# Kernel optimization log

Hardware: AMD Instinct MI355X
Metric: run time of the kernel (lower is better)

Reference implementation:

```python
import jax, jax.numpy as jnp
import numpy as np

N_HEAD = 16

def setup_inputs() -> dict:
    key = jax.random.key(0)
    ks = jax.random.split(key, 5)
    B, T, C = 4, 1024, 1024
    d = C // N_HEAD
    x = jax.random.normal(ks[0], (B, T, C), dtype=jnp.float32)
    w_attn = jax.random.normal(ks[1], (C, 3 * C), dtype=jnp.float32) * 0.02
    w_proj = jax.random.normal(ks[2], (C, C), dtype=jnp.float32) * 0.02
    embk = 0.02 * jax.random.normal(ks[3], (T, d), dtype=jnp.float32)
    embv = 0.02 * jax.random.normal(ks[4], (T, d), dtype=jnp.float32)
    return {"x": x, "w_attn": w_attn, "w_proj": w_proj, "embk": embk, "embv": embv}

def reference(x, w_attn, w_proj, embk, embv):
    B, T, C = x.shape
    H = N_HEAD
    d = C // H
    qkv = x @ w_attn                                   # [B,T,3C]
    q, k, v = jnp.split(qkv, 3, axis=2)
    q = q.reshape(B, T, H, d).transpose(0, 2, 1, 3)     # [B,H,T,d]
    k = k.reshape(B, T, H, d).transpose(0, 2, 1, 3)
    v = v.reshape(B, T, H, d).transpose(0, 2, 1, 3)
    # relative positions, lower-triangular (0 above diagonal, masked anyway)
    idx = jnp.arange(T)
    rel = jnp.tril(idx[:, None] - idx[None, :])         # [T,T] int
    rk = embk[rel]                                      # [T,T,d]
    rv = embv[rel]                                      # [T,T,d]
    scale = 1.0 / np.sqrt(d).astype(np.float32)
    att = jnp.einsum('bhtd,bhsd->bhts', q, k) * scale \
        + jnp.einsum('bhtd,tsd->bhts', q, rk)           # [B,H,T,T]
    causal = (idx[None, :] <= idx[:, None])             # [T,T] bool
    att = jnp.where(causal[None, None], att, -jnp.inf)
    att = jax.nn.softmax(att, axis=-1)
    y = jnp.einsum('bhts,bhsd->bhtd', att, v) \
      + jnp.einsum('bhts,tsd->bhtd', att, rv)           # [B,H,T,d]
    y = y.transpose(0, 2, 1, 3).reshape(B, T, C)
    return y @ w_proj
```

## Files before the change

kernel.cpp:

```cpp
#include <hip/hip_runtime.h>
#include <math.h>

typedef unsigned short u16;
typedef short bf8 __attribute__((ext_vector_type(8)));
typedef float f32x4 __attribute__((ext_vector_type(4)));

__device__ __forceinline__ u16 f2b(float f) {
    union { float f; unsigned u; } x; x.f = f;
    return (u16)((x.u + 0x7FFFu + ((x.u >> 16) & 1u)) >> 16);
}
__device__ __forceinline__ float b2f(u16 b) {
    union { unsigned u; float f; } x; x.u = ((unsigned)b) << 16;
    return x.f;
}

__device__ __forceinline__ void async16(const void* g, void* l) {
    __builtin_amdgcn_global_load_lds(
        (const __attribute__((address_space(1))) unsigned int*)g,
        (__attribute__((address_space(3))) unsigned int*)l, 16, 0, 0);
}

__device__ __forceinline__ void cstore(float* p, float v) { *p = v; }
__device__ __forceinline__ void cstore(u16* p, float v) { *p = f2b(v); }

template<typename OutT>
__global__ __launch_bounds__(256) void gemm_mfma(const u16* __restrict__ A,
                                                 const u16* __restrict__ Bt,
                                                 OutT* __restrict__ C,
                                                 int M, int N, int K) {
    __shared__ __align__(16) u16 As[128 * 32];
    __shared__ __align__(16) u16 Bs[128 * 32];
    const int tid = threadIdx.x;
    const int w = tid >> 6, L = tid & 63;
    const int l15 = L & 15, quad = L >> 4;
    const int wm = (w >> 1) * 64, wn = (w & 1) * 64;
    const int row0 = blockIdx.y * 128, col0 = blockIdx.x * 128;
    const int laneRow = L >> 2, laneCol8 = (L & 3) * 8;

    f32x4 acc[4][4] = {};

    for (int k0 = 0; k0 < K; k0 += 32) {
        #pragma unroll
        for (int i = 0; i < 2; ++i) {
            const int seg = w * 2 + i;
            const int r = seg * 16 + laneRow;
            async16(&A[(size_t)(row0 + r) * K + k0 + laneCol8], &As[seg * 512 + L * 8]);
        }
        #pragma unroll
        for (int i = 0; i < 2; ++i) {
            const int seg = w * 2 + i;
            const int r = seg * 16 + laneRow;
            async16(&Bt[(size_t)(col0 + r) * K + k0 + laneCol8], &Bs[seg * 512 + L * 8]);
        }
        __syncthreads();
        bf8 a[4], b[4];
        #pragma unroll
        for (int mt = 0; mt < 4; ++mt)
            a[mt] = *(const bf8*)&As[(wm + mt * 16 + l15) * 32 + quad * 8];
        #pragma unroll
        for (int nt = 0; nt < 4; ++nt)
            b[nt] = *(const bf8*)&Bs[(wn + nt * 16 + l15) * 32 + quad * 8];
        #pragma unroll
        for (int mt = 0; mt < 4; ++mt)
            #pragma unroll
            for (int nt = 0; nt < 4; ++nt)
                acc[mt][nt] = __builtin_amdgcn_mfma_f32_16x16x32_bf16(
                    a[mt], b[nt], acc[mt][nt], 0, 0, 0);
        __syncthreads();
    }
    #pragma unroll
    for (int mt = 0; mt < 4; ++mt)
        #pragma unroll
        for (int nt = 0; nt < 4; ++nt) {
            const int col = col0 + wn + nt * 16 + l15;
            #pragma unroll
            for (int r = 0; r < 4; ++r) {
                const int row = row0 + wm + mt * 16 + quad * 4 + r;
                cstore(&C[(size_t)row * N + col], acc[mt][nt][r]);
            }
        }
}

__global__ __launch_bounds__(256) void prep_all(const float* __restrict__ x,
                                                const float* __restrict__ embk,
                                                const float* __restrict__ embv,
                                                const float* __restrict__ w_attn,
                                                const float* __restrict__ w_proj,
                                                u16* __restrict__ xb,
                                                u16* __restrict__ EKP,
                                                u16* __restrict__ EVP,
                                                u16* __restrict__ waT,
                                                u16* __restrict__ wpT) {
    __shared__ u16 ts[64][65];
    const int bx = blockIdx.x;
    const int tid = threadIdx.x;
    if (bx < 4096) {
        int idx = bx * 256 + tid;
        const float4 v = ((const float4*)x)[idx];
        ((ushort4*)xb)[idx] = make_ushort4(f2b(v.x), f2b(v.y), f2b(v.z), f2b(v.w));
    } else if (bx < 4132) {
        int t = (bx - 4096) * 256 + tid;
        int L = t & 63, kc = (t >> 6) & 1, k16 = t >> 7;
        int l15 = L & 15, quad = L >> 4;
        int row = 1 + k16 * 16 + l15;
        int d = row - 128;
        int cl = d < 0 ? 0 : (d > 1023 ? 1023 : d);
        const float* p = embk + cl * 64 + kc * 32 + quad * 8;
        #pragma unroll
        for (int i = 0; i < 8; ++i) EKP[t * 8 + i] = f2b(p[i]);
    } else if (bx < 4168) {
        int t = (bx - 4132) * 256 + tid;
        int L = t & 63, rest = t >> 6;
        int c32 = rest % 36, tn = rest / 36;
        int l15 = L & 15, quad = L >> 4;
        #pragma unroll
        for (int i = 0; i < 8; ++i) {
            int c = c32 * 32 + quad * 8 + i;
            int d = c - 127;
            int cl = d < 0 ? 0 : (d > 1023 ? 1023 : d);
            EVP[t * 8 + i] = f2b(embv[cl * 64 + tn * 16 + l15]);
        }
    } else {
        const float* W; u16* WT; int Cc, t;
        if (bx < 4168 + 768) { t = bx - 4168; W = w_attn; WT = waT; Cc = 3072; }
        else                 { t = bx - 4936; W = w_proj; WT = wpT; Cc = 1024; }
        const int nx = Cc >> 6;
        const int c0 = (t % nx) * 64, r0 = (t / nx) * 64;
        for (int i = tid; i < 4096; i += 256) {
            int r = i >> 6, c = i & 63;
            ts[r][c] = f2b(W[(size_t)(r0 + r) * Cc + c0 + c]);
        }
        __syncthreads();
        for (int i = tid; i < 4096; i += 256) {
            int c = i >> 6, r = i & 63;
            WT[(size_t)(c0 + c) * 1024 + r0 + r] = ts[r][c];
        }
    }
}

__global__ __launch_bounds__(256) void prep_vt(const u16* __restrict__ qkvb,
                                               u16* __restrict__ Vt) {
    __shared__ u16 ts[64][65];
    const int tid = threadIdx.x;
    const int s0 = blockIdx.x * 64;
    const int bh = blockIdx.y, b = bh >> 4, h = bh & 15;
    #pragma unroll
    for (int it = 0; it < 4; ++it) {
        int s = it * 16 + (tid >> 4);
        int d4 = (tid & 15) * 4;
        const u16* p = qkvb + (size_t)(b * 1024 + s0 + s) * 3072 + 2048 + h * 64 + d4;
        #pragma unroll
        for (int i = 0; i < 4; ++i) ts[s][d4 + i] = p[i];
    }
    __syncthreads();
    const int d = tid >> 2, si = (tid & 3) * 16;
    __align__(16) u16 buf[16];
    #pragma unroll
    for (int i = 0; i < 16; ++i) buf[i] = ts[si + i][d];
    u16* o = Vt + ((size_t)(bh * 64 + d) << 10) + s0 + si;
    *(uint4*)o       = ((uint4*)buf)[0];
    *(uint4*)(o + 8) = ((uint4*)buf)[1];
}

__global__ __launch_bounds__(256) void pack_kv(const u16* __restrict__ qkvb,
                                               const u16* __restrict__ Vt,
                                               u16* __restrict__ Kp,
                                               u16* __restrict__ Vp) {
    const int bx = blockIdx.x;
    if (bx < 2048) {
        int t = bx * 256 + threadIdx.x;
        int L = t & 63, kc = (t >> 6) & 1, s16 = (t >> 7) & 63, bh = t >> 13;
        int l15 = L & 15, quad = L >> 4;
        int b = bh >> 4, h = bh & 15;
        const u16* src = qkvb + (size_t)(b * 1024 + s16 * 16 + l15) * 3072
                       + 1024 + h * 64 + kc * 32 + quad * 8;
        u16* dst = Kp + (size_t)t * 8;
        #pragma unroll
        for (int i = 0; i < 8; ++i) dst[i] = f2b(b2f(src[i]) * 0.125f);
    } else {
        int t = (bx - 2048) * 256 + threadIdx.x;
        int L = t & 63, c32 = (t >> 6) & 31, tn = (t >> 11) & 3, bh = t >> 13;
        int l15 = L & 15, quad = L >> 4;
        const u16* src = Vt + ((size_t)(bh * 64 + tn * 16 + l15) << 10)
                       + c32 * 32 + quad * 8;
        *(uint4*)(Vp + (size_t)t * 8) = *(const uint4*)src;
    }
}

__global__ __launch_bounds__(256) void attn_mfma(const u16* __restrict__ qkvb,
                                                 const u16* __restrict__ Kp,
                                                 const u16* __restrict__ Vp,
                                                 const u16* __restrict__ EKP,
                                                 const u16* __restrict__ EVP,
                                                 u16* __restrict__ yb) {
    __shared__ __align__(16) u16 slab_[4][4608];
    __shared__ __align__(16) u16 KVs[16384];

    const int tid = threadIdx.x;
    const int w = tid >> 6, L = tid & 63;
    const int l15 = L & 15, quad = L >> 4;
    const int pair = blockIdx.x;
    const int bh = blockIdx.y, b = bh >> 4, h = bh & 15;
    u16* S2l = slab_[w];
    u16* Pl  = slab_[w];
    u16* Ppl = slab_[w] + 2048;

    const bf8* EKPF = (const bf8*)EKP;
    const bf8* EVPF = (const bf8*)EVP;

    #pragma unroll 1
    for (int half = 0; half < 2; ++half) {
        const int tile = half ? pair : (15 - pair);
        const int t0 = tile * 64;

        bf8 qn[2];
        {
            const int trow = t0 + w * 16 + l15;
            const u16* qp = qkvb + (size_t)(b * 1024 + trow) * 3072 + h * 64 + quad * 8;
            qn[0] = *(const bf8*)qp;
            qn[1] = *(const bf8*)(qp + 32);
        }

        f32x4 o[4] = {};
        float lsum[4] = {0.f, 0.f, 0.f, 0.f};

        const int nch = (t0 >> 7) + 1;
        #pragma unroll 1
        for (int c = 0; c < nch; ++c) {
            const int s0 = c << 7;
            const int diff = t0 - s0;

            __syncthreads();

            {
                const size_t kbase = ((size_t)(bh * 64 + (s0 >> 4)) << 1) * 512;
                #pragma unroll
                for (int i = 0; i < 4; ++i)
                    async16(Kp + kbase + (i * 256 + tid) * 8, &KVs[(i * 256 + tid) * 8]);
                const int vb = bh * 128 + (s0 >> 5);
                #pragma unroll
                for (int i = 0; i < 4; ++i)
                    async16(Vp + ((size_t)(vb + i * 32) * 512 + tid * 8),
                            &KVs[8192 + i * 2048 + tid * 8]);
            }

            f32x4 s2[9] = {};
            {
                const int kb = (diff >> 4) + w;
                #pragma unroll
                for (int j = 0; j < 9; ++j) {
                    #pragma unroll
                    for (int kc = 0; kc < 2; ++kc)
                        s2[j] = __builtin_amdgcn_mfma_f32_16x16x32_bf16(
                            qn[kc], EKPF[(((kb + j) << 1) + kc) * 64 + L], s2[j], 0, 0, 0);
                }
            }
            #pragma unroll
            for (int j = 0; j < 9; ++j)
                #pragma unroll
                for (int r = 0; r < 4; ++r)
                    S2l[(quad * 4 + r) * 148 + j * 16 + l15] = f2b(s2[j][r]);

            __syncthreads();

            f32x4 s1[8] = {};
            #pragma unroll
            for (int tn = 0; tn < 8; ++tn) {
                #pragma unroll
                for (int kc = 0; kc < 2; ++kc) {
                    const bf8 kf = *(const bf8*)&KVs[((tn << 1) + kc) * 512 + L * 8];
                    s1[tn] = __builtin_amdgcn_mfma_f32_16x16x32_bf16(
                        qn[kc], kf, s1[tn], 0, 0, 0);
                }
            }

            #pragma unroll
            for (int tn = 0; tn < 8; ++tn) {
                const int cl = tn * 16 + l15;
                #pragma unroll
                for (int r = 0; r < 4; ++r) {
                    const int row = quad * 4 + r;
                    float v = s1[tn][r] + b2f(S2l[row * 148 + (row - cl + 127)]);
                    if (cl > diff + w * 16 + row) v = -1e30f;
                    float p = __expf(v - 4.0f);
                    s1[tn][r] = p;
                    lsum[r] += p;
                }
            }
            #pragma unroll
            for (int i = 0; i < 5; ++i)
                ((uint4*)Ppl)[i * 64 + L] = make_uint4(0, 0, 0, 0);
            #pragma unroll
            for (int tn = 0; tn < 8; ++tn) {
                const int cl = tn * 16 + l15;
                #pragma unroll
                for (int r = 0; r < 4; ++r) {
                    const int row = quad * 4 + r;
                    const u16 pb = f2b(s1[tn][r]);
                    Pl[((cl >> 5) << 9) + (((cl >> 3) & 3) << 7) + (row << 3) + (cl & 7)] = pb;
                    const int dc = (w & 1) * 16 + row - cl + 127;
                    Ppl[((dc >> 5) << 9) + (((dc >> 3) & 3) << 7) + (row << 3) + (dc & 7)] = pb;
                }
            }

            {
                bf8 pa[4];
                #pragma unroll
                for (int kc = 0; kc < 4; ++kc) pa[kc] = ((const bf8*)Pl)[kc * 64 + L];
                #pragma unroll
                for (int tn = 0; tn < 4; ++tn) {
                    #pragma unroll
                    for (int kc = 0; kc < 4; ++kc) {
                        const bf8 vf = *(const bf8*)&KVs[8192 + (tn * 4 + kc) * 512 + L * 8];
                        o[tn] = __builtin_amdgcn_mfma_f32_16x16x32_bf16(
                            pa[kc], vf, o[tn], 0, 0, 0);
                    }
                }
            }
            {
                bf8 pa[5];
                #pragma unroll
                for (int kc = 0; kc < 5; ++kc) pa[kc] = ((const bf8*)Ppl)[kc * 64 + L];
                const int eb = (diff >> 5) + (w >> 1);
                #pragma unroll
                for (int tn = 0; tn < 4; ++tn) {
                    #pragma unroll
                    for (int kc = 0; kc < 5; ++kc)
                        o[tn] = __builtin_amdgcn_mfma_f32_16x16x32_bf16(
                            pa[kc], EVPF[(tn * 36 + eb + kc) * 64 + L], o[tn], 0, 0, 0);
                }
            }
        }
        #pragma unroll
        for (int r = 0; r < 4; ++r) {
            float ls = lsum[r];
            ls += __shfl_xor(ls, 1); ls += __shfl_xor(ls, 2);
            ls += __shfl_xor(ls, 4); ls += __shfl_xor(ls, 8);
            lsum[r] = ls;
        }
        #pragma unroll
        for (int tn = 0; tn < 4; ++tn) {
            const int col = h * 64 + tn * 16 + l15;
            #pragma unroll
            for (int r = 0; r < 4; ++r) {
                const int trow = t0 + w * 16 + quad * 4 + r;
                yb[(size_t)(b * 1024 + trow) * 1024 + col] = f2b(o[tn][r] / lsum[r]);
            }
        }
    }
}

extern "C" void kernel_launch(void* const* d_in, const int* in_sizes, int n_in,
                              void* d_out, int out_size, void* d_ws, size_t ws_size,
                              hipStream_t stream) {
    const float* x      = (const float*)d_in[0];
    const float* w_attn = (const float*)d_in[1];
    const float* w_proj = (const float*)d_in[2];
    const float* embk   = (const float*)d_in[3];
    const float* embv   = (const float*)d_in[4];
    float* out = (float*)d_out;

    u16* wsb   = (u16*)d_ws;
    u16* qkvb  = wsb;
    u16* xb    = qkvb + 12582912;
    u16* ymidb = xb;
    u16* waT   = xb + 4194304;
    u16* wpT   = waT + 3145728;
    u16* Vt    = wpT + 1048576;
    u16* Kp    = Vt + 4194304;
    u16* Vp    = Kp + 4194304;
    u16* EKP   = Vp + 4194304;
    u16* EVP   = EKP + 73728;

    prep_all<<<dim3(5192), 256, 0, stream>>>(x, embk, embv, w_attn, w_proj,
                                             xb, EKP, EVP, waT, wpT);
    gemm_mfma<u16><<<dim3(24, 32), 256, 0, stream>>>(xb, waT, qkvb, 4096, 3072, 1024);
    prep_vt<<<dim3(16, 64), 256, 0, stream>>>(qkvb, Vt);
    pack_kv<<<dim3(4096), 256, 0, stream>>>(qkvb, Vt, Kp, Vp);
    attn_mfma<<<dim3(8, 64), 256, 0, stream>>>(qkvb, Kp, Vp, EKP, EVP, ymidb);
    gemm_mfma<float><<<dim3(8, 32), 256, 0, stream>>>(ymidb, wpT, out, 4096, 1024, 1024);
}
```

Baseline: 275.8 us.

## Fuse V transpose into pack_kv, use bpermute for rel-pos scores, skip masked diagonal MFMAs

Merges the prep_vt and pack_kv kernels into one that transposes V through LDS and writes the MFMA-packed Vp directly. This removes one launch and the Vt intermediate round trip through global memory. In the attention kernel, the relative-position score gather now uses ds_bpermute on registers instead of a bf16 round trip through an LDS slab, which also drops a rounding step. On diagonal chunks, MFMAs covering fully masked tiles are skipped, and the Ppl zeroing is hoisted out of the loop, with some added branching.

```diff
diff --git a/kernel.cpp b/kernel.cpp
--- a/kernel.cpp
+++ b/kernel.cpp
@@ -138,52 +138,49 @@
     }
 }
 
-__global__ __launch_bounds__(256) void prep_vt(const u16* __restrict__ qkvb,
-                                               u16* __restrict__ Vt) {
-    __shared__ u16 ts[64][65];
-    const int tid = threadIdx.x;
-    const int s0 = blockIdx.x * 64;
-    const int bh = blockIdx.y, b = bh >> 4, h = bh & 15;
-    #pragma unroll
-    for (int it = 0; it < 4; ++it) {
-        int s = it * 16 + (tid >> 4);
-        int d4 = (tid & 15) * 4;
-        const u16* p = qkvb + (size_t)(b * 1024 + s0 + s) * 3072 + 2048 + h * 64 + d4;
-        #pragma unroll
-        for (int i = 0; i < 4; ++i) ts[s][d4 + i] = p[i];
-    }
-    __syncthreads();
-    const int d = tid >> 2, si = (tid & 3) * 16;
-    __align__(16) u16 buf[16];
-    #pragma unroll
-    for (int i = 0; i < 16; ++i) buf[i] = ts[si + i][d];
-    u16* o = Vt + ((size_t)(bh * 64 + d) << 10) + s0 + si;
-    *(uint4*)o       = ((uint4*)buf)[0];
-    *(uint4*)(o + 8) = ((uint4*)buf)[1];
-}
-
 __global__ __launch_bounds__(256) void pack_kv(const u16* __restrict__ qkvb,
-                                               const u16* __restrict__ Vt,
                                                u16* __restrict__ Kp,
                                                u16* __restrict__ Vp) {
-    const int bx = blockIdx.x;
-    if (bx < 2048) {
-        int t = bx * 256 + threadIdx.x;
-        int L = t & 63, kc = (t >> 6) & 1, s16 = (t >> 7) & 63, bh = t >> 13;
-        int l15 = L & 15, quad = L >> 4;
-        int b = bh >> 4, h = bh & 15;
+    __shared__ __align__(16) u16 ts[128][72];
+    const int tid = threadIdx.x;
+    const int sb = blockIdx.x;
+    const int bh = blockIdx.y, b = bh >> 4, h = bh & 15;
+    const int s0 = sb * 128;
+    const int L = tid & 63, fr0 = tid >> 6;
+    const int l15 = L & 15, quad = L >> 4;
+
+    #pragma unroll
+    for (int it = 0; it < 2; ++it) {
+        const int row = it * 64 + (tid >> 2);
+        const int c16 = (tid & 3) * 16;
+        const u16* p = qkvb + (size_t)(b * 1024 + s0 + row) * 3072 + 2048 + h * 64 + c16;
+        *(uint4*)&ts[row][c16]     = *(const uint4*)p;
+        *(uint4*)&ts[row][c16 + 8] = *(const uint4*)(p + 8);
+    }
+    __syncthreads();
+
+    #pragma unroll
+    for (int k = 0; k < 4; ++k) {
+        const int fri = fr0 * 4 + k;
+        const int tn = fri >> 2, c32l = fri & 3;
+        const int sl = c32l * 32 + quad * 8;
+        __align__(16) u16 buf[8];
+        #pragma unroll
+        for (int i = 0; i < 8; ++i) buf[i] = ts[sl + i][tn * 16 + l15];
+        const size_t fidx = (size_t)(bh * 4 + tn) * 32 + sb * 4 + c32l;
+        *(uint4*)&Vp[fidx * 512 + L * 8] = *(uint4*)buf;
+    }
+
+    #pragma unroll
+    for (int k = 0; k < 4; ++k) {
+        const int fri = fr0 * 4 + k;
+        const int s16 = sb * 8 + (fri >> 1), kc = fri & 1;
         const u16* src = qkvb + (size_t)(b * 1024 + s16 * 16 + l15) * 3072
                        + 1024 + h * 64 + kc * 32 + quad * 8;
-        u16* dst = Kp + (size_t)t * 8;
-        #pragma unroll
-        for (int i = 0; i < 8; ++i) dst[i] = f2b(b2f(src[i]) * 0.125f);
-    } else {
-        int t = (bx - 2048) * 256 + threadIdx.x;
-        int L = t & 63, c32 = (t >> 6) & 31, tn = (t >> 11) & 3, bh = t >> 13;
-        int l15 = L & 15, quad = L >> 4;
-        const u16* src = Vt + ((size_t)(bh * 64 + tn * 16 + l15) << 10)
-                       + c32 * 32 + quad * 8;
-        *(uint4*)(Vp + (size_t)t * 8) = *(const uint4*)src;
+        __align__(16) u16 buf[8];
+        #pragma unroll
+        for (int i = 0; i < 8; ++i) buf[i] = f2b(b2f(src[i]) * 0.125f);
+        *(uint4*)&Kp[((size_t)(bh * 64 + s16) * 2 + kc) * 512 + L * 8] = *(uint4*)buf;
     }
 }
 
@@ -201,12 +198,22 @@
     const int l15 = L & 15, quad = L >> 4;
     const int pair = blockIdx.x;
     const int bh = blockIdx.y, b = bh >> 4, h = bh & 15;
-    u16* S2l = slab_[w];
     u16* Pl  = slab_[w];
     u16* Ppl = slab_[w] + 2048;
 
     const bf8* EKPF = (const bf8*)EKP;
     const bf8* EVPF = (const bf8*)EVP;
+
+    int gaddr[4];
+    #pragma unroll
+    for (int r = 0; r < 4; ++r) {
+        const int row = quad * 4 + r;
+        gaddr[r] = ((quad << 4) + ((row + 15 - l15) & 15)) << 2;
+    }
+
+    #pragma unroll
+    for (int i = 0; i < 5; ++i)
+        ((uint4*)Ppl)[i * 64 + L] = make_uint4(0, 0, 0, 0);
 
     #pragma unroll 1
     for (int half = 0; half < 2; ++half) {
@@ -229,6 +236,7 @@
         for (int c = 0; c < nch; ++c) {
             const int s0 = c << 7;
             const int diff = t0 - s0;
+            const bool dg = (diff == 0);
 
             __syncthreads();
 
@@ -249,54 +257,48 @@
                 const int kb = (diff >> 4) + w;
                 #pragma unroll
                 for (int j = 0; j < 9; ++j) {
+                    if (!(dg && j < 7 - w)) {
+                        #pragma unroll
+                        for (int kc = 0; kc < 2; ++kc)
+                            s2[j] = __builtin_amdgcn_mfma_f32_16x16x32_bf16(
+                                qn[kc], EKPF[(((kb + j) << 1) + kc) * 64 + L], s2[j], 0, 0, 0);
+                    }
+                }
+            }
+
+            __syncthreads();
+
+            f32x4 s1[8] = {};
+            #pragma unroll
+            for (int tn = 0; tn < 8; ++tn) {
+                if (!(dg && tn > w)) {
                     #pragma unroll
-                    for (int kc = 0; kc < 2; ++kc)
-                        s2[j] = __builtin_amdgcn_mfma_f32_16x16x32_bf16(
-                            qn[kc], EKPF[(((kb + j) << 1) + kc) * 64 + L], s2[j], 0, 0, 0);
-                }
-            }
-            #pragma unroll
-            for (int j = 0; j < 9; ++j)
-                #pragma unroll
-                for (int r = 0; r < 4; ++r)
-                    S2l[(quad * 4 + r) * 148 + j * 16 + l15] = f2b(s2[j][r]);
-
-            __syncthreads();
-
-            f32x4 s1[8] = {};
-            #pragma unroll
-            for (int tn = 0; tn < 8; ++tn) {
-                #pragma unroll
-                for (int kc = 0; kc < 2; ++kc) {
-                    const bf8 kf = *(const bf8*)&KVs[((tn << 1) + kc) * 512 + L * 8];
-                    s1[tn] = __builtin_amdgcn_mfma_f32_16x16x32_bf16(
-                        qn[kc], kf, s1[tn], 0, 0, 0);
-                }
-            }
-
-            #pragma unroll
-            for (int tn = 0; tn < 8; ++tn) {
-                const int cl = tn * 16 + l15;
-                #pragma unroll
-                for (int r = 0; r < 4; ++r) {
-                    const int row = quad * 4 + r;
-                    float v = s1[tn][r] + b2f(S2l[row * 148 + (row - cl + 127)]);
+                    for (int kc = 0; kc < 2; ++kc) {
+                        const bf8 kf = *(const bf8*)&KVs[((tn << 1) + kc) * 512 + L * 8];
+                        s1[tn] = __builtin_amdgcn_mfma_f32_16x16x32_bf16(
+                            qn[kc], kf, s1[tn], 0, 0, 0);
+                    }
+                }
+            }
+
+            #pragma unroll
+            for (int r = 0; r < 4; ++r) {
+                const int row = quad * 4 + r;
+                float g[9];
+                #pragma unroll
+                for (int j = 0; j < 9; ++j)
+                    g[j] = __int_as_float(__builtin_amdgcn_ds_bpermute(
+                        gaddr[r], __float_as_int(s2[j][r])));
+                const bool hi = (l15 < row);
+                #pragma unroll
+                for (int tn = 0; tn < 8; ++tn) {
+                    const int cl = tn * 16 + l15;
+                    float sv = hi ? g[8 - tn] : g[7 - tn];
+                    float v = s1[tn][r] + sv;
                     if (cl > diff + w * 16 + row) v = -1e30f;
                     float p = __expf(v - 4.0f);
-                    s1[tn][r] = p;
                     lsum[r] += p;
-                }
-            }
-            #pragma unroll
-            for (int i = 0; i < 5; ++i)
-                ((uint4*)Ppl)[i * 64 + L] = make_uint4(0, 0, 0, 0);
-            #pragma unroll
-            for (int tn = 0; tn < 8; ++tn) {
-                const int cl = tn * 16 + l15;
-                #pragma unroll
-                for (int r = 0; r < 4; ++r) {
-                    const int row = quad * 4 + r;
-                    const u16 pb = f2b(s1[tn][r]);
+                    const u16 pb = f2b(p);
                     Pl[((cl >> 5) << 9) + (((cl >> 3) & 3) << 7) + (row << 3) + (cl & 7)] = pb;
                     const int dc = (w & 1) * 16 + row - cl + 127;
                     Ppl[((dc >> 5) << 9) + (((dc >> 3) & 3) << 7) + (row << 3) + (dc & 7)] = pb;
@@ -304,30 +306,32 @@
             }
 
             {
-                bf8 pa[4];
-                #pragma unroll
-                for (int kc = 0; kc < 4; ++kc) pa[kc] = ((const bf8*)Pl)[kc * 64 + L];
-                #pragma unroll
-                for (int tn = 0; tn < 4; ++tn) {
-                    #pragma unroll
-                    for (int kc = 0; kc < 4; ++kc) {
-                        const bf8 vf = *(const bf8*)&KVs[8192 + (tn * 4 + kc) * 512 + L * 8];
-                        o[tn] = __builtin_amdgcn_mfma_f32_16x16x32_bf16(
-                            pa[kc], vf, o[tn], 0, 0, 0);
+                const int kcmax = dg ? (w >> 1) + 1 : 4;
+                #pragma unroll
+                for (int kc = 0; kc < 4; ++kc) {
+                    if (kc < kcmax) {
+                        const bf8 pa = ((const bf8*)Pl)[kc * 64 + L];
+                        #pragma unroll
+                        for (int tn = 0; tn < 4; ++tn) {
+                            const bf8 vf = *(const bf8*)&KVs[8192 + (tn * 4 + kc) * 512 + L * 8];
+                            o[tn] = __builtin_amdgcn_mfma_f32_16x16x32_bf16(
+                                pa, vf, o[tn], 0, 0, 0);
+                        }
                     }
                 }
             }
             {
-                bf8 pa[5];
-                #pragma unroll
-                for (int kc = 0; kc < 5; ++kc) pa[kc] = ((const bf8*)Ppl)[kc * 64 + L];
+                const int e0 = dg ? ((w < 2) ? 3 : 2) : 0;
                 const int eb = (diff >> 5) + (w >> 1);
                 #pragma unroll
-                for (int tn = 0; tn < 4; ++tn) {
-                    #pragma unroll
-                    for (int kc = 0; kc < 5; ++kc)
-                        o[tn] = __builtin_amdgcn_mfma_f32_16x16x32_bf16(
-                            pa[kc], EVPF[(tn * 36 + eb + kc) * 64 + L], o[tn], 0, 0, 0);
+                for (int kc = 0; kc < 5; ++kc) {
+                    if (kc >= e0) {
+                        const bf8 pa = ((const bf8*)Ppl)[kc * 64 + L];
+                        #pragma unroll
+                        for (int tn = 0; tn < 4; ++tn)
+                            o[tn] = __builtin_amdgcn_mfma_f32_16x16x32_bf16(
+                                pa, EVPF[(tn * 36 + eb + kc) * 64 + L], o[tn], 0, 0, 0);
+                    }
                 }
             }
         }
@@ -366,8 +370,7 @@
     u16* ymidb = xb;
     u16* waT   = xb + 4194304;
     u16* wpT   = waT + 3145728;
-    u16* Vt    = wpT + 1048576;
-    u16* Kp    = Vt + 4194304;
+    u16* Kp    = wpT + 1048576;
     u16* Vp    = Kp + 4194304;
     u16* EKP   = Vp + 4194304;
     u16* EVP   = EKP + 73728;
@@ -375,8 +378,7 @@
     prep_all<<<dim3(5192), 256, 0, stream>>>(x, embk, embv, w_attn, w_proj,
                                              xb, EKP, EVP, waT, wpT);
     gemm_mfma<u16><<<dim3(24, 32), 256, 0, stream>>>(xb, waT, qkvb, 4096, 3072, 1024);
-    prep_vt<<<dim3(16, 64), 256, 0, stream>>>(qkvb, Vt);
-    pack_kv<<<dim3(4096), 256, 0, stream>>>(qkvb, Vt, Kp, Vp);
+    pack_kv<<<dim3(8, 64), 256, 0, stream>>>(qkvb, Kp, Vp);
     attn_mfma<<<dim3(8, 64), 256, 0, stream>>>(qkvb, Kp, Vp, EKP, EVP, ymidb);
     gemm_mfma<float><<<dim3(8, 32), 256, 0, stream>>>(ymidb, wpT, out, 4096, 1024, 1024);
 }
```

Measured after the change: 313.0 us. 1.14x slower.
